# Optimization experiments

Measured on AMD Instinct MI355X. Metric: run time of the kernel, lower is better.

The kernel has to match this reference:

```python
import jax, jax.numpy as jnp
import numpy as np

B, F, D = 16384, 256, 128
H = [512, 256]
OUT = 8
VOCAB = 100000


def setup_inputs() -> dict:
    key = jax.random.key(0)
    ks = jax.random.split(key, 16)
    s = lambda k, *sh: jax.random.normal(k, sh, jnp.float32) * 0.05
    return dict(
        features=jax.random.normal(ks[0], (B, F), jnp.float32),
        ent_idx=jax.random.randint(ks[1], (B,), 0, VOCAB),
        target=jax.random.randint(ks[2], (B,), 0, OUT),
        Wf=s(ks[3], F, D), bf=jnp.zeros((D,), jnp.float32),
        Wu=s(ks[4], D, D), bu=jnp.zeros((D,), jnp.float32),
        w_cf=s(ks[5], D), w_fc=s(ks[6], D),
        w_ef=s(ks[7], D), w_fe=s(ks[8], D),
        b_c=jnp.zeros((1,), jnp.float32), b_e=jnp.zeros((1,), jnp.float32),
        head_tab=s(ks[9], VOCAB, D), ent_tab=s(ks[10], VOCAB, D),
        W0=s(ks[11], 2 * D, H[0]), b0=jnp.zeros((H[0],), jnp.float32),
        W1=s(ks[12], H[0], H[1]), b1=jnp.zeros((H[1],), jnp.float32),
        W2=s(ks[13], H[1], OUT), b2=jnp.zeros((OUT,), jnp.float32),
    )


def cross_compress(f, e, w_cf, w_fc, w_ef, w_fe, b_c, b_e):
    # torch code builds c = f (outer) e of shape (B,D,D) then matmuls a (D,1)
    # vector; algebraically (f e^T) w = f * (e . w), so we use the O(B*D) form.
    ew_cf = e @ w_cf  # (B,)
    fw_fc = f @ w_fc
    ew_ef = e @ w_ef
    fw_fe = f @ w_fe
    new_f = f * ew_cf[:, None] + e * fw_fc[:, None] + b_c
    new_e = f * ew_ef[:, None] + e * fw_fe[:, None] + b_e
    return new_f, new_e


def reference(features, ent_idx, target, Wf, bf, Wu, bu, w_cf, w_fc, w_ef,
              w_fe, b_c, b_e, head_tab, ent_tab, W0, b0, W1, b1, W2, b2):
    # 'rec' branch of CompanyOperationEvaluation.forward (eval mode, dropout=id)
    cf = jax.nn.relu(features @ Wf + bf)          # feature_layer
    e = ent_tab[ent_idx]                           # entity_embed lookup
    h = head_tab[ent_idx]                          # head_embed lookup (same ids)
    for _ in range(2):
        cf = jax.nn.relu(cf @ Wu + bu)             # user_low_mlp_layer
        h, e = cross_compress(h, e, w_cf, w_fc, w_ef, w_fe, b_c, b_e)
    high = jnp.concatenate([cf, e], axis=1)        # (B, 2D)
    x = jax.nn.relu(high @ W0 + b0)
    x = jax.nn.relu(x @ W1 + b1)
    x = jax.nn.relu(x @ W2 + b2)                   # pred_last_layer
    prob = jax.nn.softmax(x, axis=1)
    return (prob, target)
```

## Files before the change

### kernel.cpp

```cpp
#include <hip/hip_runtime.h>
#include <hip/hip_bf16.h>


typedef __bf16 bf16x8 __attribute__((ext_vector_type(8)));
typedef float floatx4 __attribute__((ext_vector_type(4)));

__device__ __forceinline__ unsigned short f2bf(float x) {
  unsigned int u = __builtin_bit_cast(unsigned int, x);
  u = (u + 0x7FFFu + ((u >> 16) & 1u)) >> 16;
  return (unsigned short)u;
}

__device__ __forceinline__ unsigned pack2(float a, float b) {
  return (unsigned)f2bf(a) | ((unsigned)f2bf(b) << 16);
}

__device__ __forceinline__ int sz(int row, int col) {
  return col ^ ((row & 7) << 3);
}

#define BAR_VM(N)                                                      \
  do {                                                                 \
    asm volatile("s_waitcnt vmcnt(" #N ") lgkmcnt(0)" ::: "memory");   \
    __builtin_amdgcn_s_barrier();                                      \
    __builtin_amdgcn_sched_barrier(0);                                 \
  } while (0)

__global__ __launch_bounds__(256) void prep_kernel(
    const float* __restrict__ Wf, const float* __restrict__ Wu,
    const float* __restrict__ W0, const float* __restrict__ W1,
    const float* __restrict__ W2,
    unsigned short* __restrict__ wfT, unsigned short* __restrict__ wuT,
    unsigned short* __restrict__ w0T, unsigned short* __restrict__ w1T,
    unsigned short* __restrict__ w2T) {
  __shared__ unsigned short tile[32][34];
  const int bid = blockIdx.x, tid = threadIdx.x;
  if (bid < 304) {
    int t = bid;
    const float* src; unsigned short* dst; int N, K, kt, nt;
    if (t < 32)       { src = Wf; dst = wfT; N = 128; K = 256; kt = t >> 2;       nt = t & 3; }
    else if (t < 48)  { t -= 32;  src = Wu; dst = wuT; N = 128; K = 128; kt = t >> 2; nt = t & 3; }
    else if (t < 176) { t -= 48;  src = W0; dst = w0T; N = 512; K = 256; kt = t >> 4; nt = t & 15; }
    else              { t -= 176; src = W1; dst = w1T; N = 256; K = 512; kt = t >> 3; nt = t & 7; }
    {
      int r = tid >> 3, cg = (tid & 7) * 4;
      float4 v = *(const float4*)(src + (size_t)(kt * 32 + r) * N + nt * 32 + cg);
      tile[r][cg + 0] = f2bf(v.x); tile[r][cg + 1] = f2bf(v.y);
      tile[r][cg + 2] = f2bf(v.z); tile[r][cg + 3] = f2bf(v.w);
    }
    __syncthreads();
    {
      int rp = tid >> 3, cg = (tid & 7) * 4;
      uint2 o;
      o.x = (unsigned)tile[cg + 0][rp] | ((unsigned)tile[cg + 1][rp] << 16);
      o.y = (unsigned)tile[cg + 2][rp] | ((unsigned)tile[cg + 3][rp] << 16);
      *(uint2*)(dst + (size_t)(nt * 32 + rp) * K + kt * 32 + cg) = o;
    }
  } else {
#pragma unroll
    for (int i = 0; i < 8; ++i) {
      int g = tid * 8 + i, k = g >> 3, n = g & 7;
      w2T[n * 256 + k] = f2bf(W2[g]);
    }
  }
}

template <int CPR, int LDK>
__device__ __forceinline__ void stageB(unsigned short* dstbase,
                                       const unsigned short* __restrict__ src,
                                       int tid) {
#pragma unroll
  for (int i = 0; i < 4; ++i) {
    int chunk = i * 512 + tid;
    int row = chunk / CPR, seg = chunk % CPR;
    int segl = seg ^ (row & 7);
    const unsigned short* g = src + (size_t)row * LDK + segl * 8;
    unsigned short* d = dstbase + chunk * 8;
    __builtin_amdgcn_global_load_lds((const unsigned int*)g, (unsigned int*)d,
                                     16, 0, 0);
  }
}

template <int PASS, int BK, int NROWS, int LDK>
__device__ __forceinline__ const unsigned short* srcstep(
    const unsigned short* __restrict__ s, int st) {
  return s + (size_t)(st / PASS) * NROWS * LDK + (st % PASS) * BK;
}

template <int LDA>
__device__ __forceinline__ void mstep_n(const unsigned short* A,
                                        const unsigned short* bt, int k0,
                                        floatx4* acc, int m16, int quad,
                                        int wm, int wn) {
#pragma unroll
  for (int kk = 0; kk < 128; kk += 32) {
    const int ca = k0 + kk + quad * 8;
    const int cb = kk + quad * 8;
    const int ra0 = wm * 32 + m16, ra1 = wm * 32 + 16 + m16;
    const int rb0 = wn * 32 + m16, rb1 = wn * 32 + 16 + m16;
    bf16x8 a0 = *(const bf16x8*)&A[ra0 * LDA + sz(ra0, ca)];
    bf16x8 a1 = *(const bf16x8*)&A[ra1 * LDA + sz(ra1, ca)];
    bf16x8 b0 = *(const bf16x8*)&bt[rb0 * 128 + sz(rb0, cb)];
    bf16x8 b1 = *(const bf16x8*)&bt[rb1 * 128 + sz(rb1, cb)];
    acc[0] = __builtin_amdgcn_mfma_f32_16x16x32_bf16(b0, a0, acc[0], 0, 0, 0);
    acc[1] = __builtin_amdgcn_mfma_f32_16x16x32_bf16(b1, a0, acc[1], 0, 0, 0);
    acc[2] = __builtin_amdgcn_mfma_f32_16x16x32_bf16(b0, a1, acc[2], 0, 0, 0);
    acc[3] = __builtin_amdgcn_mfma_f32_16x16x32_bf16(b1, a1, acc[3], 0, 0, 0);
  }
}

template <int LDA>
__device__ __forceinline__ void mstep_w(const unsigned short* A,
                                        const unsigned short* bt, int k0,
                                        floatx4* acc, int m16, int quad,
                                        int wm, int wn) {
#pragma unroll
  for (int kk = 0; kk < 64; kk += 32) {
    const int ca = k0 + kk + quad * 8;
    const int cb = kk + quad * 8;
    const int ra0 = wm * 32 + m16, ra1 = wm * 32 + 16 + m16;
    bf16x8 a0 = *(const bf16x8*)&A[ra0 * LDA + sz(ra0, ca)];
    bf16x8 a1 = *(const bf16x8*)&A[ra1 * LDA + sz(ra1, ca)];
    bf16x8 b[4];
#pragma unroll
    for (int ni = 0; ni < 4; ++ni) {
      int rb = wn * 64 + ni * 16 + m16;
      b[ni] = *(const bf16x8*)&bt[rb * 64 + sz(rb, cb)];
    }
#pragma unroll
    for (int ni = 0; ni < 4; ++ni) {
      acc[ni] = __builtin_amdgcn_mfma_f32_16x16x32_bf16(b[ni], a0, acc[ni], 0, 0, 0);
      acc[4 + ni] = __builtin_amdgcn_mfma_f32_16x16x32_bf16(b[ni], a1, acc[4 + ni], 0, 0, 0);
    }
  }
}

template <int T, int LDA, int PASS, int LDK>
__device__ __forceinline__ void gemm_phase_n(
    const unsigned short* A, const unsigned short* __restrict__ src,
    unsigned short* b_sh, floatx4* acc, int tid, int m16, int quad, int wm,
    int wn) {
  stageB<16, LDK>(b_sh, srcstep<PASS, 128, 128, LDK>(src, 0), tid);
  if (T > 1) {
    stageB<16, LDK>(b_sh + 16384, srcstep<PASS, 128, 128, LDK>(src, 1), tid);
    BAR_VM(4);
  } else {
    BAR_VM(0);
  }
#pragma unroll
  for (int t = 0; t < T; ++t) {
    if (t + 2 < T)
      stageB<16, LDK>(b_sh + ((t + 2) % 3) * 16384,
                      srcstep<PASS, 128, 128, LDK>(src, t + 2), tid);
    mstep_n<LDA>(A, b_sh + (t % 3) * 16384, (t % PASS) * 128,
                 acc + (t / PASS) * 4, m16, quad, wm, wn);
    if (t + 2 < T) {
      BAR_VM(4);
    } else {
      BAR_VM(0);
    }
  }
}

template <int T, int LDA, int PASS, int LDK>
__device__ __forceinline__ void gemm_phase_w(
    const unsigned short* A, const unsigned short* __restrict__ src,
    unsigned short* b_sh, floatx4* acc, int tid, int m16, int quad, int wm,
    int wn) {
  stageB<8, LDK>(b_sh, srcstep<PASS, 64, 256, LDK>(src, 0), tid);
  if (T > 1) {
    stageB<8, LDK>(b_sh + 16384, srcstep<PASS, 64, 256, LDK>(src, 1), tid);
    BAR_VM(4);
  } else {
    BAR_VM(0);
  }
#pragma unroll
  for (int t = 0; t < T; ++t) {
    if (t + 2 < T)
      stageB<8, LDK>(b_sh + ((t + 2) % 3) * 16384,
                     srcstep<PASS, 64, 256, LDK>(src, t + 2), tid);
    mstep_w<LDA>(A, b_sh + (t % 3) * 16384, (t % PASS) * 64,
                 acc + (t / PASS) * 8, m16, quad, wm, wn);
    if (t + 2 < T) {
      BAR_VM(4);
    } else {
      BAR_VM(0);
    }
  }
}

__global__ __launch_bounds__(512, 2) void fused_mlp_kernel(
    const float* __restrict__ features, const int* __restrict__ ent_idx,
    const float* __restrict__ head_tab, const float* __restrict__ ent_tab,
    const float* __restrict__ w_cf, const float* __restrict__ w_fc,
    const float* __restrict__ w_ef, const float* __restrict__ w_fe,
    const float* __restrict__ b_c, const float* __restrict__ b_e,
    const unsigned short* __restrict__ wfT,
    const unsigned short* __restrict__ wuT, const float* __restrict__ bf_,
    const float* __restrict__ bu,
    const unsigned short* __restrict__ w0T, const float* __restrict__ b0,
    const unsigned short* __restrict__ w1T, const float* __restrict__ b1,
    const unsigned short* __restrict__ w2T, const float* __restrict__ b2,
    const int* __restrict__ target, float* __restrict__ out) {
  __shared__ __align__(16) unsigned short regionA[32768];
  __shared__ __align__(16) unsigned short b_sh[3 * 16384];
  unsigned short* feat_sh = regionA;
  unsigned short* buf0 = regionA + 16384;
  unsigned short* buf1 = regionA + 24576;
  unsigned short* A_sh = regionA;
  unsigned short* x0_sh = regionA;
  unsigned short* x1_sh = b_sh;

  const int tid = threadIdx.x;
  const int r0 = blockIdx.x * 64;
  const int lane = tid & 63, wave = tid >> 6;
  const int m16 = lane & 15, quad = lane >> 4;
  const int wm = wave >> 2, wn = wave & 3;
  const int wn2 = wave & 1;
  (void)wn2;

  const int grow = tid >> 3, gpart = tid & 7;
  const int gidx = ent_idx[r0 + grow];
  const float* hp = head_tab + (size_t)gidx * 128 + gpart * 16;
  const float* ep = ent_tab + (size_t)gidx * 128 + gpart * 16;
  float4 h4[4], e4[4];
#pragma unroll
  for (int j = 0; j < 4; ++j) {
    h4[j] = *(const float4*)(hp + j * 4);
    e4[j] = *(const float4*)(ep + j * 4);
  }

#pragma unroll
  for (int i = 0; i < 4; ++i) {
    int chunk = i * 512 + tid;
    int row = chunk >> 5, c8 = (chunk & 31) * 8;
    float4 v0 = *(const float4*)(features + (size_t)(r0 + row) * 256 + c8);
    float4 v1 = *(const float4*)(features + (size_t)(r0 + row) * 256 + c8 + 4);
    uint4 o;
    o.x = pack2(v0.x, v0.y); o.y = pack2(v0.z, v0.w);
    o.z = pack2(v1.x, v1.y); o.w = pack2(v1.z, v1.w);
    *(uint4*)&feat_sh[row * 256 + sz(row, c8)] = o;
  }

  floatx4 acc[4];
#pragma unroll
  for (int j = 0; j < 4; ++j) acc[j] = (floatx4){0.f, 0.f, 0.f, 0.f};
  gemm_phase_n<2, 256, 2, 256>(feat_sh, wfT, b_sh, acc, tid, m16, quad, wm, wn);
#pragma unroll
  for (int mi = 0; mi < 2; ++mi)
#pragma unroll
    for (int ni = 0; ni < 2; ++ni) {
      int row = wm * 32 + mi * 16 + m16;
      int col = wn * 32 + ni * 16 + quad * 4;
      float4 bv = *(const float4*)(bf_ + col);
      floatx4 v = acc[mi * 2 + ni];
      uint2 o;
      o.x = pack2(fmaxf(v[0] + bv.x, 0.f), fmaxf(v[1] + bv.y, 0.f));
      o.y = pack2(fmaxf(v[2] + bv.z, 0.f), fmaxf(v[3] + bv.w, 0.f));
      *(uint2*)&buf0[row * 128 + sz(row, col)] = o;
    }

  {
    float h[16], e[16];
#pragma unroll
    for (int j = 0; j < 4; ++j) {
      h[4 * j + 0] = h4[j].x; h[4 * j + 1] = h4[j].y;
      h[4 * j + 2] = h4[j].z; h[4 * j + 3] = h4[j].w;
      e[4 * j + 0] = e4[j].x; e[4 * j + 1] = e4[j].y;
      e[4 * j + 2] = e4[j].z; e[4 * j + 3] = e4[j].w;
    }
    float wcf[16], wfc[16], wef[16], wfe[16];
#pragma unroll
    for (int jj = 0; jj < 4; ++jj) {
      *(float4*)&wcf[jj * 4] = *(const float4*)(w_cf + gpart * 16 + jj * 4);
      *(float4*)&wfc[jj * 4] = *(const float4*)(w_fc + gpart * 16 + jj * 4);
      *(float4*)&wef[jj * 4] = *(const float4*)(w_ef + gpart * 16 + jj * 4);
      *(float4*)&wfe[jj * 4] = *(const float4*)(w_fe + gpart * 16 + jj * 4);
    }
    const float bc = b_c[0], be = b_e[0];
#pragma unroll
    for (int it = 0; it < 2; ++it) {
      float d0 = 0.f, d1 = 0.f, d2 = 0.f, d3 = 0.f;
#pragma unroll
      for (int j = 0; j < 16; ++j) {
        d0 += e[j] * wcf[j]; d1 += h[j] * wfc[j];
        d2 += e[j] * wef[j]; d3 += h[j] * wfe[j];
      }
#pragma unroll
      for (int s = 1; s < 8; s <<= 1) {
        d0 += __shfl_xor(d0, s); d1 += __shfl_xor(d1, s);
        d2 += __shfl_xor(d2, s); d3 += __shfl_xor(d3, s);
      }
#pragma unroll
      for (int j = 0; j < 16; ++j) {
        float nh = h[j] * d0 + e[j] * d1 + bc;
        float ne = h[j] * d2 + e[j] * d3 + be;
        h[j] = nh; e[j] = ne;
      }
    }
    uint4 o0, o1;
    unsigned* w = (unsigned*)&o0;
#pragma unroll
    for (int j = 0; j < 4; ++j) w[j] = pack2(e[2 * j], e[2 * j + 1]);
    w = (unsigned*)&o1;
#pragma unroll
    for (int j = 0; j < 4; ++j) w[j] = pack2(e[8 + 2 * j], e[8 + 2 * j + 1]);
    const int c0 = 128 + gpart * 16;
    *(uint4*)&A_sh[grow * 256 + sz(grow, c0)] = o0;
    *(uint4*)&A_sh[grow * 256 + sz(grow, c0 + 8)] = o1;
  }

#pragma unroll
  for (int j = 0; j < 4; ++j) acc[j] = (floatx4){0.f, 0.f, 0.f, 0.f};
  gemm_phase_n<1, 128, 1, 128>(buf0, wuT, b_sh, acc, tid, m16, quad, wm, wn);
#pragma unroll
  for (int mi = 0; mi < 2; ++mi)
#pragma unroll
    for (int ni = 0; ni < 2; ++ni) {
      int row = wm * 32 + mi * 16 + m16;
      int col = wn * 32 + ni * 16 + quad * 4;
      float4 bv = *(const float4*)(bu + col);
      floatx4 v = acc[mi * 2 + ni];
      uint2 o;
      o.x = pack2(fmaxf(v[0] + bv.x, 0.f), fmaxf(v[1] + bv.y, 0.f));
      o.y = pack2(fmaxf(v[2] + bv.z, 0.f), fmaxf(v[3] + bv.w, 0.f));
      *(uint2*)&buf1[row * 128 + sz(row, col)] = o;
    }

#pragma unroll
  for (int j = 0; j < 4; ++j) acc[j] = (floatx4){0.f, 0.f, 0.f, 0.f};
  BAR_VM(0);
  mstep_n<128>(buf1, b_sh, 0, acc, m16, quad, wm, wn);
  BAR_VM(0);
#pragma unroll
  for (int mi = 0; mi < 2; ++mi)
#pragma unroll
    for (int ni = 0; ni < 2; ++ni) {
      int row = wm * 32 + mi * 16 + m16;
      int col = wn * 32 + ni * 16 + quad * 4;
      float4 bv = *(const float4*)(bu + col);
      floatx4 v = acc[mi * 2 + ni];
      uint2 o;
      o.x = pack2(fmaxf(v[0] + bv.x, 0.f), fmaxf(v[1] + bv.y, 0.f));
      o.y = pack2(fmaxf(v[2] + bv.z, 0.f), fmaxf(v[3] + bv.w, 0.f));
      *(uint2*)&A_sh[row * 256 + sz(row, col)] = o;
    }

  floatx4 acc16[16];
#pragma unroll
  for (int j = 0; j < 16; ++j) acc16[j] = (floatx4){0.f, 0.f, 0.f, 0.f};
  gemm_phase_w<8, 256, 4, 256>(A_sh, w0T, b_sh, acc16, tid, m16, quad, wm, wn);
#pragma unroll
  for (int np = 0; np < 2; ++np)
#pragma unroll
    for (int mi = 0; mi < 2; ++mi)
#pragma unroll
      for (int ni = 0; ni < 4; ++ni) {
        int row = wm * 32 + mi * 16 + m16;
        int col = np * 256 + wn * 64 + ni * 16 + quad * 4;
        float4 bv = *(const float4*)(b0 + col);
        floatx4 v = acc16[np * 8 + mi * 4 + ni];
        uint2 o;
        o.x = pack2(fmaxf(v[0] + bv.x, 0.f), fmaxf(v[1] + bv.y, 0.f));
        o.y = pack2(fmaxf(v[2] + bv.z, 0.f), fmaxf(v[3] + bv.w, 0.f));
        *(uint2*)&x0_sh[row * 512 + sz(row, col)] = o;
      }

  floatx4 acc8[8];
#pragma unroll
  for (int j = 0; j < 8; ++j) acc8[j] = (floatx4){0.f, 0.f, 0.f, 0.f};
  gemm_phase_w<8, 512, 8, 512>(x0_sh, w1T, b_sh, acc8, tid, m16, quad, wm, wn);
#pragma unroll
  for (int mi = 0; mi < 2; ++mi)
#pragma unroll
    for (int ni = 0; ni < 4; ++ni) {
      int row = wm * 32 + mi * 16 + m16;
      int col = wn * 64 + ni * 16 + quad * 4;
      float4 bv = *(const float4*)(b1 + col);
      floatx4 v = acc8[mi * 4 + ni];
      uint2 o;
      o.x = pack2(fmaxf(v[0] + bv.x, 0.f), fmaxf(v[1] + bv.y, 0.f));
      o.y = pack2(fmaxf(v[2] + bv.z, 0.f), fmaxf(v[3] + bv.w, 0.f));
      *(uint2*)&x1_sh[row * 264 + col] = o;
    }
  BAR_VM(0);

  {
    int row = tid >> 3, q = tid & 7;
    float p[8];
#pragma unroll
    for (int n = 0; n < 8; ++n) p[n] = 0.f;
#pragma unroll
    for (int jb = 0; jb < 4; ++jb) {
      bf16x8 xv = *(const bf16x8*)&x1_sh[row * 264 + q * 32 + jb * 8];
#pragma unroll
      for (int n = 0; n < 8; ++n) {
        bf16x8 wv = *(const bf16x8*)(w2T + n * 256 + q * 32 + jb * 8);
#pragma unroll
        for (int j = 0; j < 8; ++j) p[n] += (float)xv[j] * (float)wv[j];
      }
    }
#pragma unroll
    for (int s = 1; s < 8; s <<= 1)
#pragma unroll
      for (int n = 0; n < 8; ++n) p[n] += __shfl_xor(p[n], s);
    if (q == 0) {
      float mx = -1e30f;
#pragma unroll
      for (int n = 0; n < 8; ++n) {
        p[n] = fmaxf(p[n] + b2[n], 0.f);
        mx = fmaxf(mx, p[n]);
      }
      float sum = 0.f;
#pragma unroll
      for (int n = 0; n < 8; ++n) { p[n] = __expf(p[n] - mx); sum += p[n]; }
      const float inv = 1.f / sum;
      const int gr = r0 + row;
      float4 o0 = {p[0] * inv, p[1] * inv, p[2] * inv, p[3] * inv};
      float4 o1 = {p[4] * inv, p[5] * inv, p[6] * inv, p[7] * inv};
      *(float4*)(out + (size_t)gr * 8) = o0;
      *(float4*)(out + (size_t)gr * 8 + 4) = o1;
      out[16384 * 8 + gr] = (float)target[gr];
    }
  }
}

extern "C" void kernel_launch(void* const* d_in, const int* in_sizes, int n_in,
                              void* d_out, int out_size, void* d_ws, size_t ws_size,
                              hipStream_t stream) {
  const float* features = (const float*)d_in[0];
  const int* ent_idx    = (const int*)d_in[1];
  const int* target     = (const int*)d_in[2];
  const float* Wf  = (const float*)d_in[3];
  const float* bf_ = (const float*)d_in[4];
  const float* Wu  = (const float*)d_in[5];
  const float* bu  = (const float*)d_in[6];
  const float* w_cf = (const float*)d_in[7];
  const float* w_fc = (const float*)d_in[8];
  const float* w_ef = (const float*)d_in[9];
  const float* w_fe = (const float*)d_in[10];
  const float* b_c  = (const float*)d_in[11];
  const float* b_e  = (const float*)d_in[12];
  const float* head_tab = (const float*)d_in[13];
  const float* ent_tab  = (const float*)d_in[14];
  const float* W0 = (const float*)d_in[15];
  const float* b0 = (const float*)d_in[16];
  const float* W1 = (const float*)d_in[17];
  const float* b1 = (const float*)d_in[18];
  const float* W2 = (const float*)d_in[19];
  const float* b2 = (const float*)d_in[20];
  float* out = (float*)d_out;

  unsigned short* ws = (unsigned short*)d_ws;
  size_t off = 0;
  auto alloc = [&](size_t n) { unsigned short* p = ws + off; off += n; return p; };
  unsigned short* wfT  = alloc(32768);
  unsigned short* wuT  = alloc(16384);
  unsigned short* w0T  = alloc(131072);
  unsigned short* w1T  = alloc(131072);
  unsigned short* w2T  = alloc(2048);
  (void)ws_size; (void)in_sizes; (void)n_in; (void)out_size;

  prep_kernel<<<305, 256, 0, stream>>>(Wf, Wu, W0, W1, W2,
                                       wfT, wuT, w0T, w1T, w2T);
  fused_mlp_kernel<<<256, 512, 0, stream>>>(features, ent_idx, head_tab,
      ent_tab, w_cf, w_fc, w_ef, w_fe, b_c, b_e, wfT, wuT, bf_, bu,
      w0T, b0, w1T, b1, w2T, b2, target, out);
}
```

Before: 179.5 us.

## Pipeline weight staging continuously across all GEMM phases of fused MLP

Replaces the per-phase GEMM helpers, each of which restarted its own prefetch pipeline and drained fully at phase boundaries, with one continuous triple-buffered schedule. The next phase's weight tiles (Wu, W0, W1) are prefetched while the current phase computes, including during the cross-compress and epilogue sections. This hides global-to-LDS load latency at phase transitions. In exchange, buffer-rotation indexing and vmcnt accounting become hand-coded and fragile, and the extra barriers could allow races if any count is wrong.

Result: no change. 181.9 us (+1.3%).

```diff
diff --git a/kernel.cpp b/kernel.cpp
--- a/kernel.cpp
+++ b/kernel.cpp
@@ -81,12 +81,6 @@
   }
 }
 
-template <int PASS, int BK, int NROWS, int LDK>
-__device__ __forceinline__ const unsigned short* srcstep(
-    const unsigned short* __restrict__ s, int st) {
-  return s + (size_t)(st / PASS) * NROWS * LDK + (st % PASS) * BK;
-}
-
 template <int LDA>
 __device__ __forceinline__ void mstep_n(const unsigned short* A,
                                         const unsigned short* bt, int k0,
@@ -131,60 +125,6 @@
     for (int ni = 0; ni < 4; ++ni) {
       acc[ni] = __builtin_amdgcn_mfma_f32_16x16x32_bf16(b[ni], a0, acc[ni], 0, 0, 0);
       acc[4 + ni] = __builtin_amdgcn_mfma_f32_16x16x32_bf16(b[ni], a1, acc[4 + ni], 0, 0, 0);
-    }
-  }
-}
-
-template <int T, int LDA, int PASS, int LDK>
-__device__ __forceinline__ void gemm_phase_n(
-    const unsigned short* A, const unsigned short* __restrict__ src,
-    unsigned short* b_sh, floatx4* acc, int tid, int m16, int quad, int wm,
-    int wn) {
-  stageB<16, LDK>(b_sh, srcstep<PASS, 128, 128, LDK>(src, 0), tid);
-  if (T > 1) {
-    stageB<16, LDK>(b_sh + 16384, srcstep<PASS, 128, 128, LDK>(src, 1), tid);
-    BAR_VM(4);
-  } else {
-    BAR_VM(0);
-  }
-#pragma unroll
-  for (int t = 0; t < T; ++t) {
-    if (t + 2 < T)
-      stageB<16, LDK>(b_sh + ((t + 2) % 3) * 16384,
-                      srcstep<PASS, 128, 128, LDK>(src, t + 2), tid);
-    mstep_n<LDA>(A, b_sh + (t % 3) * 16384, (t % PASS) * 128,
-                 acc + (t / PASS) * 4, m16, quad, wm, wn);
-    if (t + 2 < T) {
-      BAR_VM(4);
-    } else {
-      BAR_VM(0);
-    }
-  }
-}
-
-template <int T, int LDA, int PASS, int LDK>
-__device__ __forceinline__ void gemm_phase_w(
-    const unsigned short* A, const unsigned short* __restrict__ src,
-    unsigned short* b_sh, floatx4* acc, int tid, int m16, int quad, int wm,
-    int wn) {
-  stageB<8, LDK>(b_sh, srcstep<PASS, 64, 256, LDK>(src, 0), tid);
-  if (T > 1) {
-    stageB<8, LDK>(b_sh + 16384, srcstep<PASS, 64, 256, LDK>(src, 1), tid);
-    BAR_VM(4);
-  } else {
-    BAR_VM(0);
-  }
-#pragma unroll
-  for (int t = 0; t < T; ++t) {
-    if (t + 2 < T)
-      stageB<8, LDK>(b_sh + ((t + 2) % 3) * 16384,
-                     srcstep<PASS, 64, 256, LDK>(src, t + 2), tid);
-    mstep_w<LDA>(A, b_sh + (t % 3) * 16384, (t % PASS) * 64,
-                 acc + (t / PASS) * 8, m16, quad, wm, wn);
-    if (t + 2 < T) {
-      BAR_VM(4);
-    } else {
-      BAR_VM(0);
     }
   }
 }
@@ -205,19 +145,18 @@
   __shared__ __align__(16) unsigned short regionA[32768];
   __shared__ __align__(16) unsigned short b_sh[3 * 16384];
   unsigned short* feat_sh = regionA;
-  unsigned short* buf0 = regionA + 16384;
-  unsigned short* buf1 = regionA + 24576;
+  unsigned short* rbuf0 = regionA + 16384;
+  unsigned short* rbuf1 = regionA + 24576;
   unsigned short* A_sh = regionA;
   unsigned short* x0_sh = regionA;
   unsigned short* x1_sh = b_sh;
+  unsigned short* B[3] = {b_sh, b_sh + 16384, b_sh + 32768};
 
   const int tid = threadIdx.x;
   const int r0 = blockIdx.x * 64;
   const int lane = tid & 63, wave = tid >> 6;
   const int m16 = lane & 15, quad = lane >> 4;
   const int wm = wave >> 2, wn = wave & 3;
-  const int wn2 = wave & 1;
-  (void)wn2;
 
   const int grow = tid >> 3, gpart = tid & 7;
   const int gidx = ent_idx[r0 + grow];
@@ -242,10 +181,20 @@
     *(uint4*)&feat_sh[row * 256 + sz(row, c8)] = o;
   }
 
-  floatx4 acc[4];
-#pragma unroll
-  for (int j = 0; j < 4; ++j) acc[j] = (floatx4){0.f, 0.f, 0.f, 0.f};
-  gemm_phase_n<2, 256, 2, 256>(feat_sh, wfT, b_sh, acc, tid, m16, quad, wm, wn);
+  stageB<16, 256>(B[0], wfT, tid);
+  stageB<16, 256>(B[1], wfT + 128, tid);
+  BAR_VM(4);
+
+  floatx4 accL[4];
+#pragma unroll
+  for (int j = 0; j < 4; ++j) accL[j] = (floatx4){0.f, 0.f, 0.f, 0.f};
+  stageB<16, 128>(B[2], wuT, tid);
+  mstep_n<256>(feat_sh, B[0], 0, accL, m16, quad, wm, wn);
+  BAR_VM(4);
+  stageB<8, 256>(B[0], w0T, tid);
+  mstep_n<256>(feat_sh, B[1], 128, accL, m16, quad, wm, wn);
+  BAR_VM(4);
+
 #pragma unroll
   for (int mi = 0; mi < 2; ++mi)
 #pragma unroll
@@ -253,13 +202,12 @@
       int row = wm * 32 + mi * 16 + m16;
       int col = wn * 32 + ni * 16 + quad * 4;
       float4 bv = *(const float4*)(bf_ + col);
-      floatx4 v = acc[mi * 2 + ni];
+      floatx4 v = accL[mi * 2 + ni];
       uint2 o;
       o.x = pack2(fmaxf(v[0] + bv.x, 0.f), fmaxf(v[1] + bv.y, 0.f));
       o.y = pack2(fmaxf(v[2] + bv.z, 0.f), fmaxf(v[3] + bv.w, 0.f));
-      *(uint2*)&buf0[row * 128 + sz(row, col)] = o;
-    }
-
+      *(uint2*)&rbuf0[row * 128 + sz(row, col)] = o;
+    }
   {
     float h[16], e[16];
 #pragma unroll
@@ -309,10 +257,14 @@
     *(uint4*)&A_sh[grow * 256 + sz(grow, c0)] = o0;
     *(uint4*)&A_sh[grow * 256 + sz(grow, c0 + 8)] = o1;
   }
-
-#pragma unroll
-  for (int j = 0; j < 4; ++j) acc[j] = (floatx4){0.f, 0.f, 0.f, 0.f};
-  gemm_phase_n<1, 128, 1, 128>(buf0, wuT, b_sh, acc, tid, m16, quad, wm, wn);
+  BAR_VM(4);
+
+  floatx4 accM[4];
+#pragma unroll
+  for (int j = 0; j < 4; ++j) accM[j] = (floatx4){0.f, 0.f, 0.f, 0.f};
+  stageB<8, 256>(B[1], w0T + 64, tid);
+  mstep_n<128>(rbuf0, B[2], 0, accM, m16, quad, wm, wn);
+  BAR_VM(4);
 #pragma unroll
   for (int mi = 0; mi < 2; ++mi)
 #pragma unroll
@@ -320,18 +272,17 @@
       int row = wm * 32 + mi * 16 + m16;
       int col = wn * 32 + ni * 16 + quad * 4;
       float4 bv = *(const float4*)(bu + col);
-      floatx4 v = acc[mi * 2 + ni];
+      floatx4 v = accM[mi * 2 + ni];
       uint2 o;
       o.x = pack2(fmaxf(v[0] + bv.x, 0.f), fmaxf(v[1] + bv.y, 0.f));
       o.y = pack2(fmaxf(v[2] + bv.z, 0.f), fmaxf(v[3] + bv.w, 0.f));
-      *(uint2*)&buf1[row * 128 + sz(row, col)] = o;
-    }
-
-#pragma unroll
-  for (int j = 0; j < 4; ++j) acc[j] = (floatx4){0.f, 0.f, 0.f, 0.f};
-  BAR_VM(0);
-  mstep_n<128>(buf1, b_sh, 0, acc, m16, quad, wm, wn);
-  BAR_VM(0);
+      *(uint2*)&rbuf1[row * 128 + sz(row, col)] = o;
+    }
+  BAR_VM(4);
+#pragma unroll
+  for (int j = 0; j < 4; ++j) accM[j] = (floatx4){0.f, 0.f, 0.f, 0.f};
+  mstep_n<128>(rbuf1, B[2], 0, accM, m16, quad, wm, wn);
+  BAR_VM(4);
 #pragma unroll
   for (int mi = 0; mi < 2; ++mi)
 #pragma unroll
@@ -339,17 +290,30 @@
       int row = wm * 32 + mi * 16 + m16;
       int col = wn * 32 + ni * 16 + quad * 4;
       float4 bv = *(const float4*)(bu + col);
-      floatx4 v = acc[mi * 2 + ni];
+      floatx4 v = accM[mi * 2 + ni];
       uint2 o;
       o.x = pack2(fmaxf(v[0] + bv.x, 0.f), fmaxf(v[1] + bv.y, 0.f));
       o.y = pack2(fmaxf(v[2] + bv.z, 0.f), fmaxf(v[3] + bv.w, 0.f));
       *(uint2*)&A_sh[row * 256 + sz(row, col)] = o;
     }
+  BAR_VM(4);
 
   floatx4 acc16[16];
 #pragma unroll
   for (int j = 0; j < 16; ++j) acc16[j] = (floatx4){0.f, 0.f, 0.f, 0.f};
-  gemm_phase_w<8, 256, 4, 256>(A_sh, w0T, b_sh, acc16, tid, m16, quad, wm, wn);
+#pragma unroll
+  for (int i = 0; i < 8; ++i) {
+    if (i <= 5) {
+      stageB<8, 256>(B[(i + 5) % 3],
+                     w0T + (size_t)((2 + i) / 4) * 65536 + ((2 + i) % 4) * 64,
+                     tid);
+    } else {
+      stageB<8, 512>(B[(i + 5) % 3], w1T + (i - 6) * 64, tid);
+    }
+    mstep_w<256>(A_sh, B[(3 + i) % 3], (i % 4) * 64, acc16 + (i / 4) * 8, m16,
+                 quad, wm, wn);
+    BAR_VM(4);
+  }
 #pragma unroll
   for (int np = 0; np < 2; ++np)
 #pragma unroll
@@ -365,11 +329,23 @@
         o.y = pack2(fmaxf(v[2] + bv.z, 0.f), fmaxf(v[3] + bv.w, 0.f));
         *(uint2*)&x0_sh[row * 512 + sz(row, col)] = o;
       }
+  BAR_VM(4);
 
   floatx4 acc8[8];
 #pragma unroll
   for (int j = 0; j < 8; ++j) acc8[j] = (floatx4){0.f, 0.f, 0.f, 0.f};
-  gemm_phase_w<8, 512, 8, 512>(x0_sh, w1T, b_sh, acc8, tid, m16, quad, wm, wn);
+#pragma unroll
+  for (int j = 0; j < 8; ++j) {
+    if (j <= 5) {
+      stageB<8, 512>(B[(j + 13) % 3], w1T + (j + 2) * 64, tid);
+    }
+    mstep_w<512>(x0_sh, B[(11 + j) % 3], j * 64, acc8, m16, quad, wm, wn);
+    if (j < 6) {
+      BAR_VM(4);
+    } else {
+      BAR_VM(0);
+    }
+  }
 #pragma unroll
   for (int mi = 0; mi < 2; ++mi)
 #pragma unroll
```
